# Kernel tuning notes

Measured on AMD Instinct MI355X. Metric: run time of the kernel, lower is better.

Reference implementation:

```python
import jax, jax.numpy as jnp
import numpy as np

N_NODES = 50000
N_EDGES = 1600000
NODE_DIM = 64
HID = 16


def setup_inputs() -> dict:
    key = jax.random.key(0)
    ks = jax.random.split(key, 12)
    f = lambda k, shape: (jax.random.normal(k, shape, dtype=jnp.float32) * 0.1)
    edge_index = jax.random.randint(ks[0], (2, N_EDGES), 0, N_NODES)
    return {
        "edge_index": edge_index,
        "node_emb": f(ks[1], (N_NODES, NODE_DIM)),
        "edge_emb": f(ks[2], (N_EDGES, HID)),
        "W1": f(ks[3], (NODE_DIM, HID)),
        "att_src1": f(ks[4], (HID,)),
        "att_dst1": f(ks[5], (HID,)),
        "b1": jnp.zeros((HID,), jnp.float32),
        "W2": f(ks[6], (HID, HID)),
        "att_src2": f(ks[7], (HID,)),
        "att_dst2": f(ks[8], (HID,)),
        "b2": jnp.zeros((HID,), jnp.float32),
        "Wm1": f(ks[9], (3 * HID, HID)),
        "bm1": jnp.zeros((HID,), jnp.float32),
        "Wm2": f(ks[10], (HID, 1)),
        "bm2": jnp.zeros((1,), jnp.float32),
    }


def gat_layer(x, src, dst, W, a_src, a_dst, b, num_nodes):
    # Single-head GATConv (PyG defaults): self-loops, leaky_relu(0.2), softmax over dst.
    h = x @ W  # [N, out]
    logits = jax.nn.leaky_relu((h @ a_src)[src] + (h @ a_dst)[dst], negative_slope=0.2)
    m = jax.ops.segment_max(logits, dst, num_segments=num_nodes)  # stable softmax
    e = jnp.exp(logits - jax.lax.stop_gradient(m)[dst])
    denom = jax.ops.segment_sum(e, dst, num_segments=num_nodes)
    coef = e / denom[dst]  # [E+N]
    out = jax.ops.segment_sum(coef[:, None] * h[src], dst, num_segments=num_nodes)
    return out + b


def reference(edge_index, node_emb, edge_emb, W1, att_src1, att_dst1, b1,
              W2, att_src2, att_dst2, b2, Wm1, bm1, Wm2, bm2):
    src, dst = edge_index[0], edge_index[1]
    num_nodes = node_emb.shape[0]
    loops = jnp.arange(num_nodes)
    src_f = jnp.concatenate([src, loops])  # GATConv add_self_loops=True
    dst_f = jnp.concatenate([dst, loops])

    x = node_emb
    for (W, a_s, a_d, b) in [(W1, att_src1, att_dst1, b1), (W2, att_src2, att_dst2, b2)]:
        x = gat_layer(x, src_f, dst_f, W, a_s, a_d, b, num_nodes)
        x = jax.nn.gelu(x, approximate=False)  # torch F.gelu default = exact erf
        # dropout omitted (eval mode)

    # Vectorized replacement of the per-edge Python loop:
    edge_repr = jnp.concatenate([x[src], x[dst], edge_emb], axis=1)  # [E, 3*HID]
    hmid = jax.nn.relu(edge_repr @ Wm1 + bm1)
    probs = jax.nn.sigmoid(hmid @ Wm2 + bm2)[:, 0]  # [E]
    return probs
```

## Files before the change

kernel.cpp:

```cpp
#include <hip/hip_runtime.h>
#include <math.h>

#define N_NODES 50000
#define N_EDGES 1600000
#define NODE_DIM 64
#define HID 16
#define BSZ 64
#define NBUCK ((N_NODES + BSZ - 1) / BSZ)
#define CAPB 2560
#define EPB 8192
#define APB 256
#define APPEND_BLOCKS ((N_EDGES + EPB - 1) / EPB)

__global__ void append_kernel(const int* __restrict__ ei,
                              int* __restrict__ gcount,
                              unsigned int* __restrict__ blist) {
    __shared__ int lcount[NBUCK];
    __shared__ int gbase[NBUCK];
    __shared__ int loff[NBUCK];
    int t = threadIdx.x;
    for (int b = t; b < NBUCK; b += APB) { lcount[b] = 0; loff[b] = 0; }
    __syncthreads();
    long base = (long)blockIdx.x * EPB;
#pragma unroll
    for (int k = 0; k < EPB / APB; k++) {
        long i = base + k * APB + t;
        if (i < N_EDGES) atomicAdd(&lcount[ei[N_EDGES + i] >> 6], 1);
    }
    __syncthreads();
    for (int b = t; b < NBUCK; b += APB) {
        int c = lcount[b];
        gbase[b] = c ? atomicAdd(&gcount[b], c) : 0;
    }
    __syncthreads();
#pragma unroll
    for (int k = 0; k < EPB / APB; k++) {
        long i = base + k * APB + t;
        if (i < N_EDGES) {
            int s = ei[i], d = ei[N_EDGES + i];
            int b = d >> 6;
            int pos = gbase[b] + atomicAdd(&loff[b], 1);
            if (pos < CAPB)
                blist[(size_t)b * CAPB + pos] = ((unsigned)(d & 63) << 16) | (unsigned)s;
        }
    }
}

__global__ void sort_kernel(const int* __restrict__ gcount, const unsigned int* __restrict__ blist,
                            unsigned short* __restrict__ csr, int* __restrict__ dstbeg) {
    __shared__ int cnts[BSZ];
    __shared__ int sc[BSZ];
    __shared__ int off[BSZ];
    int b = blockIdx.x, t = threadIdx.x;
    if (t < BSZ) cnts[t] = 0;
    __syncthreads();
    int cnt = gcount[b]; if (cnt > CAPB) cnt = CAPB;
    const unsigned int* lp = blist + (size_t)b * CAPB;
    for (int k = t; k < cnt; k += APB) atomicAdd(&cnts[lp[k] >> 16], 1);
    __syncthreads();
    if (t < BSZ) sc[t] = cnts[t];
    __syncthreads();
    for (int o = 1; o < BSZ; o <<= 1) {
        int v = 0;
        if (t < BSZ && t >= o) v = sc[t - o];
        __syncthreads();
        if (t < BSZ) sc[t] += v;
        __syncthreads();
    }
    if (t < BSZ) {
        int beg = sc[t] - cnts[t];
        off[t] = beg;
        dstbeg[(b << 6) + t] = beg;
    }
    __syncthreads();
    for (int k = t; k < cnt; k += APB) {
        unsigned int r = lp[k];
        int pos = atomicAdd(&off[r >> 16], 1);
        csr[(size_t)b * CAPB + pos] = (unsigned short)(r & 0xFFFF);
    }
}

__global__ void node_h64(const float* __restrict__ x,
                         const float* __restrict__ W,
                         const float* __restrict__ a_src,
                         const float* __restrict__ a_dst,
                         float* __restrict__ h,
                         float* __restrict__ as_, float* __restrict__ ad_) {
    __shared__ float Ws[NODE_DIM * HID];
    __shared__ float asv[HID], adv[HID];
    int t = threadIdx.x;
    for (int i = t; i < NODE_DIM * HID; i += blockDim.x) Ws[i] = W[i];
    if (t < HID) { asv[t] = a_src[t]; adv[t] = a_dst[t]; }
    __syncthreads();
    int n = blockIdx.x * blockDim.x + t;
    if (n >= N_NODES) return;
    float acc[HID];
#pragma unroll
    for (int j = 0; j < HID; j++) acc[j] = 0.f;
    const float4* xr = (const float4*)(x + (size_t)n * NODE_DIM);
#pragma unroll
    for (int k4 = 0; k4 < NODE_DIM / 4; k4++) {
        float4 xv = xr[k4];
        const float* w0 = Ws + (k4 * 4) * HID;
#pragma unroll
        for (int j = 0; j < HID; j++)
            acc[j] += xv.x * w0[j] + xv.y * w0[HID + j] + xv.z * w0[2 * HID + j] + xv.w * w0[3 * HID + j];
    }
    float s = 0.f, d = 0.f;
#pragma unroll
    for (int j = 0; j < HID; j++) {
        h[(size_t)n * HID + j] = acc[j];
        s += acc[j] * asv[j];
        d += acc[j] * adv[j];
    }
    as_[n] = s; ad_[n] = d;
}

__global__ void node_h16(const float* __restrict__ x,
                         const float* __restrict__ W,
                         const float* __restrict__ a_src,
                         const float* __restrict__ a_dst,
                         float* __restrict__ h,
                         float* __restrict__ as_, float* __restrict__ ad_) {
    __shared__ float Ws[HID * HID];
    __shared__ float asv[HID], adv[HID];
    int t = threadIdx.x;
    for (int i = t; i < HID * HID; i += blockDim.x) Ws[i] = W[i];
    if (t < HID) { asv[t] = a_src[t]; adv[t] = a_dst[t]; }
    __syncthreads();
    int n = blockIdx.x * blockDim.x + t;
    if (n >= N_NODES) return;
    float acc[HID];
#pragma unroll
    for (int j = 0; j < HID; j++) acc[j] = 0.f;
    const float* xr = x + (size_t)n * HID;
#pragma unroll
    for (int k = 0; k < HID; k++) {
        float xv = xr[k];
#pragma unroll
        for (int j = 0; j < HID; j++) acc[j] += xv * Ws[k * HID + j];
    }
    float s = 0.f, d = 0.f;
#pragma unroll
    for (int j = 0; j < HID; j++) {
        h[(size_t)n * HID + j] = acc[j];
        s += acc[j] * asv[j];
        d += acc[j] * adv[j];
    }
    as_[n] = s; ad_[n] = d;
}

__global__ void gather_kernel(const int* __restrict__ gcount, const int* __restrict__ dstbeg,
                              const unsigned short* __restrict__ csr,
                              const float* __restrict__ h,
                              const float* __restrict__ as_, const float* __restrict__ ad_,
                              const float* __restrict__ b,
                              float* __restrict__ xout) {
    int g = blockIdx.x * (blockDim.x >> 4) + (threadIdx.x >> 4);
    int j = threadIdx.x & 15;
    if (g >= N_NODES) return;
    int bk = g >> 6, dl = g & 63;
    int cnt_b = gcount[bk]; if (cnt_b > CAPB) cnt_b = CAPB;
    int beg = dstbeg[g];
    int end = (dl < 63) ? dstbeg[g + 1] : cnt_b;
    if (end > cnt_b) end = cnt_b;
    if (beg > end) beg = end;
    const unsigned short* row = csr + (size_t)bk * CAPB + beg;
    int cnt = end - beg;
    float adn = ad_[g];
    float acc = 0.f, den = 0.f;
    int k = 0;
    for (; k + 2 <= cnt; k += 2) {
        int s0 = row[k], s1 = row[k + 1];
        float l0 = as_[s0] + adn, l1 = as_[s1] + adn;
        l0 = l0 > 0.f ? l0 : 0.2f * l0;
        l1 = l1 > 0.f ? l1 : 0.2f * l1;
        float e0 = expf(l0), e1 = expf(l1);
        float h0 = h[(size_t)s0 * HID + j], h1 = h[(size_t)s1 * HID + j];
        den += e0 + e1;
        acc += e0 * h0 + e1 * h1;
    }
    if (k < cnt) {
        int s = row[k];
        float lg = as_[s] + adn;
        lg = lg > 0.f ? lg : 0.2f * lg;
        float e = expf(lg);
        den += e;
        acc += e * h[(size_t)s * HID + j];
    }
    float lg = as_[g] + adn;
    lg = lg > 0.f ? lg : 0.2f * lg;
    float e = expf(lg);
    den += e;
    acc += e * h[(size_t)g * HID + j];
    float v = acc / den + b[j];
    xout[(size_t)g * HID + j] = 0.5f * v * (1.f + erff(v * 0.70710678118654752f));
}

__global__ void edge_mlp(const int* __restrict__ ei,
                         const float* __restrict__ x,
                         const float* __restrict__ ee,
                         const float* __restrict__ Wm1,
                         const float* __restrict__ bm1,
                         const float* __restrict__ Wm2,
                         const float* __restrict__ bm2,
                         float* __restrict__ out) {
    __shared__ float W1s[48 * HID];
    __shared__ float b1s[HID], W2s[HID];
    __shared__ float b2s;
    int t = threadIdx.x;
    for (int i = t; i < 48 * HID; i += blockDim.x) W1s[i] = Wm1[i];
    if (t < HID) { b1s[t] = bm1[t]; W2s[t] = Wm2[t]; }
    if (t == 0) b2s = bm2[0];
    __syncthreads();
    long i = (long)blockIdx.x * blockDim.x + t;
    if (i >= N_EDGES) return;
    int s = ei[i], d = ei[N_EDGES + i];
    float in[48];
    const float4* xs = (const float4*)(x + (size_t)s * HID);
    const float4* xd = (const float4*)(x + (size_t)d * HID);
    const float4* ep = (const float4*)(ee + (size_t)i * HID);
#pragma unroll
    for (int q = 0; q < 4; q++) {
        float4 v = xs[q];
        in[4*q] = v.x; in[4*q+1] = v.y; in[4*q+2] = v.z; in[4*q+3] = v.w;
    }
#pragma unroll
    for (int q = 0; q < 4; q++) {
        float4 v = xd[q];
        in[HID+4*q] = v.x; in[HID+4*q+1] = v.y; in[HID+4*q+2] = v.z; in[HID+4*q+3] = v.w;
    }
#pragma unroll
    for (int q = 0; q < 4; q++) {
        float4 v = ep[q];
        in[2*HID+4*q] = v.x; in[2*HID+4*q+1] = v.y; in[2*HID+4*q+2] = v.z; in[2*HID+4*q+3] = v.w;
    }
    float o = b2s;
#pragma unroll
    for (int j = 0; j < HID; j++) {
        float acc = b1s[j];
#pragma unroll
        for (int k = 0; k < 48; k++) acc += in[k] * W1s[k * HID + j];
        acc = fmaxf(acc, 0.f);
        o += acc * W2s[j];
    }
    float p = 1.f / (1.f + expf(-o));
    out[i] = p;
}

extern "C" void kernel_launch(void* const* d_in, const int* in_sizes, int n_in,
                              void* d_out, int out_size, void* d_ws, size_t ws_size,
                              hipStream_t stream) {
    const int*   ei       = (const int*)d_in[0];
    const float* node_emb = (const float*)d_in[1];
    const float* edge_emb = (const float*)d_in[2];
    const float* W1       = (const float*)d_in[3];
    const float* att_src1 = (const float*)d_in[4];
    const float* att_dst1 = (const float*)d_in[5];
    const float* b1       = (const float*)d_in[6];
    const float* W2       = (const float*)d_in[7];
    const float* att_src2 = (const float*)d_in[8];
    const float* att_dst2 = (const float*)d_in[9];
    const float* b2       = (const float*)d_in[10];
    const float* Wm1      = (const float*)d_in[11];
    const float* bm1      = (const float*)d_in[12];
    const float* Wm2      = (const float*)d_in[13];
    const float* bm2      = (const float*)d_in[14];
    float* out            = (float*)d_out;

    char* w = (char*)d_ws;
    float*          h      = (float*)w;          w += (size_t)N_NODES * HID * 4;
    float*          xcur   = (float*)w;          w += (size_t)N_NODES * HID * 4;
    float*          as_    = (float*)w;          w += (size_t)N_NODES * 4;
    float*          ad_    = (float*)w;          w += (size_t)N_NODES * 4;
    int*            gcount = (int*)w;            w += (size_t)NBUCK * 4;
    unsigned int*   blist  = (unsigned int*)w;   w += (size_t)NBUCK * CAPB * 4;
    unsigned short* csr    = (unsigned short*)w; w += (size_t)NBUCK * CAPB * 2;
    int*            dstbeg = (int*)w;            w += (size_t)NBUCK * BSZ * 4;

    const int BT = 256;
    int nblk_node = (N_NODES + BT - 1) / BT;
    int nblk_E    = (N_EDGES + BT - 1) / BT;
    int nblk_g    = (N_NODES * HID + BT - 1) / BT;

    hipMemsetAsync(gcount, 0, (size_t)NBUCK * sizeof(int), stream);
    append_kernel<<<APPEND_BLOCKS, APB, 0, stream>>>(ei, gcount, blist);
    sort_kernel<<<NBUCK, APB, 0, stream>>>(gcount, blist, csr, dstbeg);

    node_h64<<<nblk_node, BT, 0, stream>>>(node_emb, W1, att_src1, att_dst1, h, as_, ad_);
    gather_kernel<<<nblk_g, BT, 0, stream>>>(gcount, dstbeg, csr, h, as_, ad_, b1, xcur);

    node_h16<<<nblk_node, BT, 0, stream>>>(xcur, W2, att_src2, att_dst2, h, as_, ad_);
    gather_kernel<<<nblk_g, BT, 0, stream>>>(gcount, dstbeg, csr, h, as_, ad_, b2, xcur);

    edge_mlp<<<nblk_E, BT, 0, stream>>>(ei, xcur, edge_emb, Wm1, bm1, Wm2, bm2, out);
}
```

Measured before the change: 373.1 us.

## Precompute per-node MLP projections and unroll gather loop by four

The first MLP layer is linear over the concatenated [x_src, x_dst, edge_emb] input, so the x_src and x_dst parts are now computed once per node (A = x@Wa + b, B = x@Wb) in a new edge_prep kernel. The per-edge kernel then adds A[src] + B[dst] and only does the 16x16 edge_emb product, cutting per-edge FLOPs to about a third. A and B are stored in the now-unused blist workspace. The GAT gather loop is also unrolled from two edges per step to four to expose more memory-level parallelism. This adds one extra launch and changes floating-point summation order.

After: 375.7 us. No clear change (+0.7%).

```diff
diff --git a/kernel.cpp b/kernel.cpp
--- a/kernel.cpp
+++ b/kernel.cpp
@@ -170,17 +170,21 @@
     float adn = ad_[g];
     float acc = 0.f, den = 0.f;
     int k = 0;
-    for (; k + 2 <= cnt; k += 2) {
-        int s0 = row[k], s1 = row[k + 1];
+    for (; k + 4 <= cnt; k += 4) {
+        int s0 = row[k], s1 = row[k + 1], s2 = row[k + 2], s3 = row[k + 3];
         float l0 = as_[s0] + adn, l1 = as_[s1] + adn;
+        float l2 = as_[s2] + adn, l3 = as_[s3] + adn;
         l0 = l0 > 0.f ? l0 : 0.2f * l0;
         l1 = l1 > 0.f ? l1 : 0.2f * l1;
-        float e0 = expf(l0), e1 = expf(l1);
+        l2 = l2 > 0.f ? l2 : 0.2f * l2;
+        l3 = l3 > 0.f ? l3 : 0.2f * l3;
+        float e0 = expf(l0), e1 = expf(l1), e2 = expf(l2), e3 = expf(l3);
         float h0 = h[(size_t)s0 * HID + j], h1 = h[(size_t)s1 * HID + j];
-        den += e0 + e1;
-        acc += e0 * h0 + e1 * h1;
-    }
-    if (k < cnt) {
+        float h2 = h[(size_t)s2 * HID + j], h3 = h[(size_t)s3 * HID + j];
+        den += (e0 + e1) + (e2 + e3);
+        acc += (e0 * h0 + e1 * h1) + (e2 * h2 + e3 * h3);
+    }
+    for (; k < cnt; k++) {
         int s = row[k];
         float lg = as_[s] + adn;
         lg = lg > 0.f ? lg : 0.2f * lg;
@@ -197,55 +201,101 @@
     xout[(size_t)g * HID + j] = 0.5f * v * (1.f + erff(v * 0.70710678118654752f));
 }
 
+__global__ void edge_prep(const float* __restrict__ x,
+                          const float* __restrict__ Wm1,
+                          const float* __restrict__ bm1,
+                          float* __restrict__ A,
+                          float* __restrict__ B) {
+    __shared__ float Wa[HID * HID];
+    __shared__ float Wb[HID * HID];
+    __shared__ float bs[HID];
+    int t = threadIdx.x;
+    for (int i = t; i < HID * HID; i += blockDim.x) {
+        Wa[i] = Wm1[i];
+        Wb[i] = Wm1[HID * HID + i];
+    }
+    if (t < HID) bs[t] = bm1[t];
+    __syncthreads();
+    int n = blockIdx.x * blockDim.x + t;
+    if (n >= N_NODES) return;
+    float xr[HID];
+    const float4* xp = (const float4*)(x + (size_t)n * HID);
+#pragma unroll
+    for (int q = 0; q < 4; q++) {
+        float4 v = xp[q];
+        xr[4 * q] = v.x; xr[4 * q + 1] = v.y; xr[4 * q + 2] = v.z; xr[4 * q + 3] = v.w;
+    }
+    float a[HID], bb[HID];
+#pragma unroll
+    for (int j = 0; j < HID; j++) { a[j] = bs[j]; bb[j] = 0.f; }
+#pragma unroll
+    for (int k = 0; k < HID; k++) {
+        float xv = xr[k];
+#pragma unroll
+        for (int j = 0; j < HID; j++) {
+            a[j]  += xv * Wa[k * HID + j];
+            bb[j] += xv * Wb[k * HID + j];
+        }
+    }
+    float4* Ap = (float4*)(A + (size_t)n * HID);
+    float4* Bp = (float4*)(B + (size_t)n * HID);
+#pragma unroll
+    for (int q = 0; q < 4; q++) {
+        Ap[q] = make_float4(a[4 * q], a[4 * q + 1], a[4 * q + 2], a[4 * q + 3]);
+        Bp[q] = make_float4(bb[4 * q], bb[4 * q + 1], bb[4 * q + 2], bb[4 * q + 3]);
+    }
+}
+
 __global__ void edge_mlp(const int* __restrict__ ei,
-                         const float* __restrict__ x,
+                         const float* __restrict__ A,
+                         const float* __restrict__ B,
                          const float* __restrict__ ee,
                          const float* __restrict__ Wm1,
-                         const float* __restrict__ bm1,
                          const float* __restrict__ Wm2,
                          const float* __restrict__ bm2,
                          float* __restrict__ out) {
-    __shared__ float W1s[48 * HID];
-    __shared__ float b1s[HID], W2s[HID];
+    __shared__ float We[HID * HID];
+    __shared__ float W2s[HID];
     __shared__ float b2s;
     int t = threadIdx.x;
-    for (int i = t; i < 48 * HID; i += blockDim.x) W1s[i] = Wm1[i];
-    if (t < HID) { b1s[t] = bm1[t]; W2s[t] = Wm2[t]; }
+    for (int i = t; i < HID * HID; i += blockDim.x) We[i] = Wm1[2 * HID * HID + i];
+    if (t < HID) W2s[t] = Wm2[t];
     if (t == 0) b2s = bm2[0];
     __syncthreads();
     long i = (long)blockIdx.x * blockDim.x + t;
     if (i >= N_EDGES) return;
     int s = ei[i], d = ei[N_EDGES + i];
-    float in[48];
-    const float4* xs = (const float4*)(x + (size_t)s * HID);
-    const float4* xd = (const float4*)(x + (size_t)d * HID);
+    float a[HID];
+    const float4* Ap = (const float4*)(A + (size_t)s * HID);
+    const float4* Bp = (const float4*)(B + (size_t)d * HID);
+#pragma unroll
+    for (int q = 0; q < 4; q++) {
+        float4 av = Ap[q]; float4 bv = Bp[q];
+        a[4 * q]     = av.x + bv.x;
+        a[4 * q + 1] = av.y + bv.y;
+        a[4 * q + 2] = av.z + bv.z;
+        a[4 * q + 3] = av.w + bv.w;
+    }
     const float4* ep = (const float4*)(ee + (size_t)i * HID);
+    const float4* W4 = (const float4*)We;
 #pragma unroll
     for (int q = 0; q < 4; q++) {
-        float4 v = xs[q];
-        in[4*q] = v.x; in[4*q+1] = v.y; in[4*q+2] = v.z; in[4*q+3] = v.w;
-    }
-#pragma unroll
-    for (int q = 0; q < 4; q++) {
-        float4 v = xd[q];
-        in[HID+4*q] = v.x; in[HID+4*q+1] = v.y; in[HID+4*q+2] = v.z; in[HID+4*q+3] = v.w;
-    }
-#pragma unroll
-    for (int q = 0; q < 4; q++) {
-        float4 v = ep[q];
-        in[2*HID+4*q] = v.x; in[2*HID+4*q+1] = v.y; in[2*HID+4*q+2] = v.z; in[2*HID+4*q+3] = v.w;
+        float4 ev = ep[q];
+#pragma unroll
+        for (int r = 0; r < 4; r++) {
+            int k = 4 * q + r;
+            float e1 = (r == 0) ? ev.x : (r == 1) ? ev.y : (r == 2) ? ev.z : ev.w;
+            float4 w0 = W4[k * 4 + 0], w1 = W4[k * 4 + 1], w2 = W4[k * 4 + 2], w3 = W4[k * 4 + 3];
+            a[0]  += e1 * w0.x; a[1]  += e1 * w0.y; a[2]  += e1 * w0.z; a[3]  += e1 * w0.w;
+            a[4]  += e1 * w1.x; a[5]  += e1 * w1.y; a[6]  += e1 * w1.z; a[7]  += e1 * w1.w;
+            a[8]  += e1 * w2.x; a[9]  += e1 * w2.y; a[10] += e1 * w2.z; a[11] += e1 * w2.w;
+            a[12] += e1 * w3.x; a[13] += e1 * w3.y; a[14] += e1 * w3.z; a[15] += e1 * w3.w;
+        }
     }
     float o = b2s;
 #pragma unroll
-    for (int j = 0; j < HID; j++) {
-        float acc = b1s[j];
-#pragma unroll
-        for (int k = 0; k < 48; k++) acc += in[k] * W1s[k * HID + j];
-        acc = fmaxf(acc, 0.f);
-        o += acc * W2s[j];
-    }
-    float p = 1.f / (1.f + expf(-o));
-    out[i] = p;
+    for (int j = 0; j < HID; j++) o += fmaxf(a[j], 0.f) * W2s[j];
+    out[i] = 1.f / (1.f + expf(-o));
 }
 
 extern "C" void kernel_launch(void* const* d_in, const int* in_sizes, int n_in,
@@ -278,6 +328,9 @@
     unsigned short* csr    = (unsigned short*)w; w += (size_t)NBUCK * CAPB * 2;
     int*            dstbeg = (int*)w;            w += (size_t)NBUCK * BSZ * 4;
 
+    float* Anode = (float*)blist;
+    float* Bnode = Anode + (size_t)N_NODES * HID;
+
     const int BT = 256;
     int nblk_node = (N_NODES + BT - 1) / BT;
     int nblk_E    = (N_EDGES + BT - 1) / BT;
@@ -293,5 +346,6 @@
     node_h16<<<nblk_node, BT, 0, stream>>>(xcur, W2, att_src2, att_dst2, h, as_, ad_);
     gather_kernel<<<nblk_g, BT, 0, stream>>>(gcount, dstbeg, csr, h, as_, ad_, b2, xcur);
 
-    edge_mlp<<<nblk_E, BT, 0, stream>>>(ei, xcur, edge_emb, Wm1, bm1, Wm2, bm2, out);
-}
+    edge_prep<<<nblk_node, BT, 0, stream>>>(xcur, Wm1, bm1, Anode, Bnode);
+    edge_mlp<<<nblk_E, BT, 0, stream>>>(ei, Anode, Bnode, edge_emb, Wm1, Wm2, bm2, out);
+}
```
